# Kernel tuning notes

Measured on AMD Instinct MI355X. Metric: run time of the kernel, lower is better.

Reference implementation:

```python
import jax, jax.numpy as jnp
import numpy as np

N = 50000
E = 800000
IN_DIM = 128
HID = 32
HEADS = 8
OUT_DIM = 64
BN_EPS = 1e-5
NEG_SLOPE = 0.2


def batch_norm(x, gamma, beta, mean, var):
    # eval-mode BatchNorm1d using running statistics
    return (x - mean) * jax.lax.rsqrt(var + BN_EPS) * gamma + beta


def gat_conv(x, src, dst, W, att_src, att_dst, heads, out_ch, n):
    """PyG GATConv (shared src/dst lin), self-loops already included in src/dst.
    x: [n, in]; W: [in, heads*out_ch]; att_*: [heads, out_ch].
    Returns [n, heads, out_ch]."""
    h = (x @ W).reshape(n, heads, out_ch)                       # node features per head
    a_s = jnp.einsum('nho,ho->nh', h, att_src)                  # [n, heads]
    a_d = jnp.einsum('nho,ho->nh', h, att_dst)
    e = jax.nn.leaky_relu(a_s[src] + a_d[dst], NEG_SLOPE)       # [e, heads]
    # segment softmax over incoming edges of each dst node
    mx = jax.ops.segment_max(e, dst, num_segments=n)
    ex = jnp.exp(e - mx[dst])
    denom = jax.ops.segment_sum(ex, dst, num_segments=n)
    alpha = ex / (denom[dst] + 1e-16)                           # [e, heads]
    out = jax.ops.segment_sum(alpha[:, :, None] * h[src], dst, num_segments=n)
    return out                                                  # [n, heads, out_ch]


def setup_inputs() -> dict:
    key = jax.random.key(0)
    ks = jax.random.split(key, 24)
    inp = {}
    inp['x'] = jax.random.normal(ks[0], (N, IN_DIM), dtype=jnp.float32)
    inp['edge_index'] = jax.random.randint(ks[1], (2, E), 0, N, dtype=jnp.int64)
    s = 0.05
    inp['W1'] = jax.random.normal(ks[2], (IN_DIM, HEADS * HID), dtype=jnp.float32) * s
    inp['a_src1'] = jax.random.normal(ks[3], (HEADS, HID), dtype=jnp.float32) * s
    inp['a_dst1'] = jax.random.normal(ks[4], (HEADS, HID), dtype=jnp.float32) * s
    inp['b1'] = jnp.zeros((HEADS * HID,), dtype=jnp.float32)
    inp['W2'] = jax.random.normal(ks[5], (HEADS * HID, OUT_DIM), dtype=jnp.float32) * s
    inp['a_src2'] = jax.random.normal(ks[6], (1, OUT_DIM), dtype=jnp.float32) * s
    inp['a_dst2'] = jax.random.normal(ks[7], (1, OUT_DIM), dtype=jnp.float32) * s
    inp['b2'] = jnp.zeros((OUT_DIM,), dtype=jnp.float32)
    # projection Linear(out_dim -> in_dim)
    inp['Wp'] = jax.random.normal(ks[8], (OUT_DIM, IN_DIM), dtype=jnp.float32) * s
    inp['bp'] = jnp.zeros((IN_DIM,), dtype=jnp.float32)
    # BatchNorm params (eval mode running stats)
    for i, d in [(1, HEADS * HID), (2, OUT_DIM), (3, IN_DIM)]:
        k0, k1, k2, k3 = jax.random.split(ks[8 + i], 4)
        inp[f'g{i}'] = 1.0 + 0.1 * jax.random.normal(k0, (d,), dtype=jnp.float32)
        inp[f'be{i}'] = 0.1 * jax.random.normal(k1, (d,), dtype=jnp.float32)
        inp[f'm{i}'] = 0.1 * jax.random.normal(k2, (d,), dtype=jnp.float32)
        inp[f'v{i}'] = jax.random.uniform(k3, (d,), dtype=jnp.float32, minval=0.5, maxval=1.5)
    return inp


def reference(x, edge_index, W1, a_src1, a_dst1, b1, W2, a_src2, a_dst2, b2,
              Wp, bp, g1, be1, m1, v1, g2, be2, m2, v2, g3, be3, m3, v3):
    n = x.shape[0]
    loops = jnp.arange(n, dtype=edge_index.dtype)
    src = jnp.concatenate([edge_index[0], loops])   # add_self_loops=True (PyG default)
    dst = jnp.concatenate([edge_index[1], loops])

    h = gat_conv(x, src, dst, W1, a_src1, a_dst1, HEADS, HID, n)
    h = h.reshape(n, HEADS * HID) + b1              # concat=True
    h = jax.nn.elu(batch_norm(h, g1, be1, m1, v1))  # dropout is no-op in eval

    h = gat_conv(h, src, dst, W2, a_src2, a_dst2, 1, OUT_DIM, n)
    h = h.reshape(n, OUT_DIM) + b2                  # concat=False, heads=1 -> mean == identity
    h = jax.nn.elu(batch_norm(h, g2, be2, m2, v2))

    h = h @ Wp + bp
    return batch_norm(h, g3, be3, m3, v3)
```

## Files before the change

kernel.cpp:

```cpp
#include <hip/hip_runtime.h>
#include <math.h>

#define NEG_SLOPE 0.2f
#define BN_EPS 1e-5f

typedef __bf16 bf16x8 __attribute__((ext_vector_type(8)));
typedef float  f32x4  __attribute__((ext_vector_type(4)));

__device__ __forceinline__ float elu_f(float x){ return x > 0.f ? x : expm1f(x); }
__device__ __forceinline__ float lrelu_f(float x){ return x > 0.f ? x : NEG_SLOPE * x; }

__device__ __forceinline__ float b2f(ushort u){
    union { uint i; float f; } v; v.i = (uint)u << 16; return v.f;
}
__device__ __forceinline__ ushort f2b(float f){
    union { float f; uint i; } v; v.f = f;
    uint r = v.i + 0x7FFFu + ((v.i >> 16) & 1u);
    return (ushort)(r >> 16);
}

__device__ __forceinline__ bool detect_f64(const void* ei, int E, long long N)
{
    const long long* p = (const long long*)ei;
    int lane = threadIdx.x & 63;
    long long v = p[lane % max(1, min(2 * E, 64))];
    bool bad = (v < 0 || v >= N);
    return __ballot(bad) == 0ull;
}

__device__ __forceinline__ void get_edge(const void* ei, int e, int E, bool f64, int& s, int& d)
{
    if (e < E) {
        if (f64) { const long long* p = (const long long*)ei; s = (int)p[e]; d = (int)p[E + e]; }
        else     { const int*       p = (const int*)ei;       s = p[e];      d = p[E + e]; }
    } else {
        s = d = e - E;
    }
}

__global__ void setup_kernel(const void* ei, int E, int N, int* deg,
    const float* __restrict__ W1, const float* __restrict__ W2, const float* __restrict__ Wp,
    ushort* __restrict__ wt1, ushort* __restrict__ wt2, ushort* __restrict__ wtp,
    const float* b1, const float* b2, const float* bp,
    const float* g1, const float* be1, const float* m1, const float* v1,
    const float* g2, const float* be2, const float* m2, const float* v2,
    const float* g3, const float* be3, const float* m3, const float* v3,
    float* par)
{
    int b = blockIdx.x, t = threadIdx.x;
    if (b == 0) {
        { float s = g1[t] * rsqrtf(v1[t] + BN_EPS); par[t] = s;        par[256 + t] = b1[t] * s + be1[t] - m1[t] * s; }
        if (t < 64)  { float s = g2[t] * rsqrtf(v2[t] + BN_EPS); par[512 + t] = s;  par[576 + t] = b2[t] * s + be2[t] - m2[t] * s; }
        if (t < 128) { float s = g3[t] * rsqrtf(v3[t] + BN_EPS); par[640 + t] = s;  par[768 + t] = bp[t] * s + be3[t] - m3[t] * s; }
    } else if (b <= 224) {
        int idx = (b - 1) * 256 + t;
        if (idx < 32768) {
            int n = idx >> 7, k = idx & 127;
            wt1[idx] = f2b(W1[k * 256 + n]);
        } else if (idx < 49152) {
            int j = idx - 32768;
            int n = j >> 8, k = j & 255;
            wt2[j] = f2b(W2[k * 64 + n]);
        } else if (idx < 57344) {
            int j = idx - 49152;
            int n = j >> 6, k = j & 63;
            wtp[j] = f2b(Wp[k * 128 + n]);
        }
    } else {
        bool f64 = detect_f64(ei, E, (long long)N);
        int i = (b - 225) * 256 + t;
        int ET = E + N;
        if (i < ET) {
            int s, d;
            get_edge(ei, i, E, f64, s, d);
            atomicAdd(&deg[d], 1);
        }
    }
}

__global__ void scan1_kernel(const int* __restrict__ deg, int N, int* __restrict__ bsum)
{
    int b = blockIdx.x, t = threadIdx.x;
    int base = b * 4096 + t * 16;
    int s = 0;
    #pragma unroll
    for (int k = 0; k < 16; k += 4) {
        int idx = base + k;
        if (idx + 3 < N) {
            int4 v = *reinterpret_cast<const int4*>(&deg[idx]);
            s += v.x + v.y + v.z + v.w;
        } else {
            for (int q = 0; q < 4; ++q) if (idx + q < N) s += deg[idx + q];
        }
    }
    #pragma unroll
    for (int off = 1; off < 64; off <<= 1) s += __shfl_xor(s, off);
    __shared__ int wsum[4];
    if ((t & 63) == 0) wsum[t >> 6] = s;
    __syncthreads();
    if (t == 0) bsum[b] = wsum[0] + wsum[1] + wsum[2] + wsum[3];
}

__global__ void scan2_kernel(const int* __restrict__ bsum, int nb, int* __restrict__ bpre)
{
    if (threadIdx.x == 0) {
        int r = 0;
        for (int i = 0; i < nb; ++i) { bpre[i] = r; r += bsum[i]; }
        bpre[nb] = r;
    }
}

__global__ void scan3_kernel(const int* __restrict__ deg, int N,
                             const int* __restrict__ bpre, int nb,
                             int* __restrict__ rowptr, int* __restrict__ fillptr)
{
    int b = blockIdx.x, t = threadIdx.x;
    int base = b * 4096 + t * 16;
    int loc[16];
    int s = 0;
    #pragma unroll
    for (int k = 0; k < 16; ++k) {
        int idx = base + k;
        int d = (idx < N) ? deg[idx] : 0;
        loc[k] = s; s += d;
    }
    int lane = t & 63;
    int incl = s;
    #pragma unroll
    for (int off = 1; off < 64; off <<= 1) {
        int v = __shfl_up(incl, off);
        if (lane >= off) incl += v;
    }
    __shared__ int wsum[4];
    if (lane == 63) wsum[t >> 6] = incl;
    __syncthreads();
    int woff = 0;
    int w = t >> 6;
    for (int i = 0; i < w; ++i) woff += wsum[i];
    int off0 = bpre[b] + woff + incl - s;
    #pragma unroll
    for (int k = 0; k < 16; ++k) {
        int idx = base + k;
        if (idx < N) { rowptr[idx] = off0 + loc[k]; fillptr[idx] = off0 + loc[k]; }
    }
    if (b == 0 && t == 0) rowptr[N] = bpre[nb];
}

__global__ void fill_kernel(const void* ei, int E, int N, int* fillptr, int* esrc)
{
    bool f64 = detect_f64(ei, E, (long long)N);
    int i = blockIdx.x * blockDim.x + threadIdx.x;
    int ET = E + N;
    if (i >= ET) return;
    int s, d;
    get_edge(ei, i, E, f64, s, d);
    int pos = atomicAdd(&fillptr[d], 1);
    esrc[pos] = s;
}

template<int ATYPE, int OMODE, int ATT>
__global__ __launch_bounds__(256) void mgemm_kernel(const void* __restrict__ Ap,
    const ushort* __restrict__ Bt, void* __restrict__ Cp, int M, int K, int NC,
    const float* __restrict__ S, const float* __restrict__ Cc,
    const float* __restrict__ att_s, const float* __restrict__ att_d,
    float* __restrict__ as_out, float* __restrict__ ad_out)
{
    const int BM = 128, LDA = 72;
    __shared__ __align__(16) ushort As[BM][LDA];
    __shared__ __align__(16) ushort Bs[64][LDA];
    __shared__ float red[128][2];
    int t = threadIdx.x;
    int m0 = blockIdx.x * BM, n0 = blockIdx.y * 64;
    int w = t >> 6, l = t & 63;
    int wm = w >> 1, wn = w & 1;
    int r16 = l & 15, kg = l >> 4;

    f32x4 acc[4][2];
    #pragma unroll
    for (int mi = 0; mi < 4; ++mi)
        #pragma unroll
        for (int ni = 0; ni < 2; ++ni)
            acc[mi][ni] = (f32x4){0.f, 0.f, 0.f, 0.f};

    for (int kb = 0; kb < K; kb += 64) {
        if (ATYPE == 0) {
            const float* A = (const float*)Ap;
            #pragma unroll
            for (int p = 0; p < 8; ++p) {
                int r = (t >> 4) + p * 16, c4 = (t & 15) * 4;
                int gm = m0 + r;
                float4 v = (gm < M) ? *reinterpret_cast<const float4*>(&A[(size_t)gm * K + kb + c4])
                                    : make_float4(0.f, 0.f, 0.f, 0.f);
                ushort4 u; u.x = f2b(v.x); u.y = f2b(v.y); u.z = f2b(v.z); u.w = f2b(v.w);
                *reinterpret_cast<ushort4*>(&As[r][c4]) = u;
            }
        } else {
            const ushort* A = (const ushort*)Ap;
            #pragma unroll
            for (int p = 0; p < 4; ++p) {
                int r = (t >> 3) + p * 32, c8 = (t & 7) * 8;
                int gm = m0 + r;
                uint4 v = (gm < M) ? *reinterpret_cast<const uint4*>(&A[(size_t)gm * K + kb + c8])
                                   : make_uint4(0u, 0u, 0u, 0u);
                *reinterpret_cast<uint4*>(&As[r][c8]) = v;
            }
        }
        #pragma unroll
        for (int p = 0; p < 2; ++p) {
            int r = (t >> 3) + p * 32, c8 = (t & 7) * 8;
            uint4 v = *reinterpret_cast<const uint4*>(&Bt[(size_t)(n0 + r) * K + kb + c8]);
            *reinterpret_cast<uint4*>(&Bs[r][c8]) = v;
        }
        __syncthreads();
        #pragma unroll
        for (int kk = 0; kk < 2; ++kk) {
            bf16x8 bB[2], bA[4];
            #pragma unroll
            for (int ni = 0; ni < 2; ++ni)
                bB[ni] = *reinterpret_cast<const bf16x8*>(&Bs[wn * 32 + ni * 16 + r16][kk * 32 + kg * 8]);
            #pragma unroll
            for (int mi = 0; mi < 4; ++mi)
                bA[mi] = *reinterpret_cast<const bf16x8*>(&As[wm * 64 + mi * 16 + r16][kk * 32 + kg * 8]);
            #pragma unroll
            for (int mi = 0; mi < 4; ++mi)
                #pragma unroll
                for (int ni = 0; ni < 2; ++ni)
                    acc[mi][ni] = __builtin_amdgcn_mfma_f32_16x16x32_bf16(bA[mi], bB[ni], acc[mi][ni], 0, 0, 0);
        }
        __syncthreads();
    }
    #pragma unroll
    for (int mi = 0; mi < 4; ++mi) {
        #pragma unroll
        for (int ni = 0; ni < 2; ++ni) {
            #pragma unroll
            for (int rg = 0; rg < 4; ++rg) {
                int gm = m0 + wm * 64 + mi * 16 + kg * 4 + rg;
                int gc = n0 + wn * 32 + ni * 16 + r16;
                if (gm < M) {
                    float v = acc[mi][ni][rg];
                    if (OMODE == 0) ((ushort*)Cp)[(size_t)gm * NC + gc] = f2b(v);
                    else            ((float*)Cp)[(size_t)gm * NC + gc] = v * S[gc] + Cc[gc];
                }
            }
        }
    }
    if (ATT) {
        float cs0 = att_s[n0 + wn * 32 + r16], cs1 = att_s[n0 + wn * 32 + 16 + r16];
        float cd0 = att_d[n0 + wn * 32 + r16], cd1 = att_d[n0 + wn * 32 + 16 + r16];
        float sp[4][4], dp[4][4];
        #pragma unroll
        for (int mi = 0; mi < 4; ++mi)
            #pragma unroll
            for (int rg = 0; rg < 4; ++rg) {
                sp[mi][rg] = acc[mi][0][rg] * cs0 + acc[mi][1][rg] * cs1;
                dp[mi][rg] = acc[mi][0][rg] * cd0 + acc[mi][1][rg] * cd1;
            }
        #pragma unroll
        for (int off = 1; off < 16; off <<= 1)
            #pragma unroll
            for (int mi = 0; mi < 4; ++mi)
                #pragma unroll
                for (int rg = 0; rg < 4; ++rg) {
                    sp[mi][rg] += __shfl_xor(sp[mi][rg], off);
                    dp[mi][rg] += __shfl_xor(dp[mi][rg], off);
                }
        if (ATT == 1) {
            int head = (n0 >> 5) + wn;
            if (r16 == 0) {
                #pragma unroll
                for (int mi = 0; mi < 4; ++mi)
                    #pragma unroll
                    for (int rg = 0; rg < 4; ++rg) {
                        int gm = m0 + wm * 64 + mi * 16 + kg * 4 + rg;
                        if (gm < M) {
                            as_out[gm * 8 + head] = sp[mi][rg];
                            ad_out[gm * 8 + head] = dp[mi][rg];
                        }
                    }
            }
        } else {
            if (wn == 1 && r16 == 0) {
                #pragma unroll
                for (int mi = 0; mi < 4; ++mi)
                    #pragma unroll
                    for (int rg = 0; rg < 4; ++rg) {
                        int r = wm * 64 + mi * 16 + kg * 4 + rg;
                        red[r][0] = sp[mi][rg];
                        red[r][1] = dp[mi][rg];
                    }
            }
            __syncthreads();
            if (wn == 0 && r16 == 0) {
                #pragma unroll
                for (int mi = 0; mi < 4; ++mi)
                    #pragma unroll
                    for (int rg = 0; rg < 4; ++rg) {
                        int r = wm * 64 + mi * 16 + kg * 4 + rg;
                        int gm = m0 + r;
                        if (gm < M) {
                            as_out[gm] = sp[mi][rg] + red[r][0];
                            ad_out[gm] = dp[mi][rg] + red[r][1];
                        }
                    }
            }
        }
    }
}

__global__ void agg1_kernel(const ushort* __restrict__ h1,
                            const float* __restrict__ as1, const float* __restrict__ ad1,
                            const int* __restrict__ rowptr, const int* __restrict__ esrc,
                            const float* __restrict__ par,
                            ushort* __restrict__ outb, int N)
{
    __shared__ float wlds_all[4][64 * 8];
    float* wlds = wlds_all[threadIdx.x >> 6];
    int wid = (blockIdx.x * blockDim.x + threadIdx.x) >> 6;
    int lane = threadIdx.x & 63;
    if (wid >= N) return;
    int beg = rowptr[wid], end = rowptr[wid + 1];
    int h = lane & 7, j = lane >> 3;
    int li = lane & 31, half = lane >> 5, hh = li >> 2;
    float ad_h = ad1[wid * 8 + h];
    float den = 0.f;
    float acc[8] = {0.f, 0.f, 0.f, 0.f, 0.f, 0.f, 0.f, 0.f};

    for (int cb = beg; cb < end; cb += 64) {
        int ce = min(cb + 64, end);
        for (int i = cb + j; i < ce; i += 8) {
            float wv = __expf(lrelu_f(as1[esrc[i] * 8 + h] + ad_h));
            wlds[(i - cb) * 8 + h] = wv;
            den += wv;
        }
        __builtin_amdgcn_wave_barrier();
        auto edge1 = [&](int ii) {
            int src = esrc[ii];
            float al = wlds[(ii - cb) * 8 + hh];
            uint4 r = *reinterpret_cast<const uint4*>(&h1[(size_t)src * 256 + li * 8]);
            union { uint u; float f; } c0, c1;
            c0.u = r.x << 16; c1.u = r.x & 0xffff0000u; acc[0] += al * c0.f; acc[1] += al * c1.f;
            c0.u = r.y << 16; c1.u = r.y & 0xffff0000u; acc[2] += al * c0.f; acc[3] += al * c1.f;
            c0.u = r.z << 16; c1.u = r.z & 0xffff0000u; acc[4] += al * c0.f; acc[5] += al * c1.f;
            c0.u = r.w << 16; c1.u = r.w & 0xffff0000u; acc[6] += al * c0.f; acc[7] += al * c1.f;
        };
        int i = cb + half;
        for (; i + 6 < ce; i += 8) { edge1(i); edge1(i + 2); edge1(i + 4); edge1(i + 6); }
        for (; i < ce; i += 2) edge1(i);
        __builtin_amdgcn_wave_barrier();
    }

    den += __shfl_xor(den, 8, 64);
    den += __shfl_xor(den, 16, 64);
    den += __shfl_xor(den, 32, 64);
    float inv = 1.f / (den + 1e-16f);
    float inv_h = __shfl(inv, hh, 64);

    #pragma unroll
    for (int f = 0; f < 8; ++f) acc[f] += __shfl_xor(acc[f], 32, 64);
    if (half == 0) {
        int f0 = li * 8;
        const float* S1 = par;
        const float* C1 = par + 256;
        ushort o[8];
        #pragma unroll
        for (int f = 0; f < 8; ++f) o[f] = f2b(elu_f(acc[f] * inv_h * S1[f0 + f] + C1[f0 + f]));
        uint4 pk;
        pk.x = (uint)o[0] | ((uint)o[1] << 16);
        pk.y = (uint)o[2] | ((uint)o[3] << 16);
        pk.z = (uint)o[4] | ((uint)o[5] << 16);
        pk.w = (uint)o[6] | ((uint)o[7] << 16);
        *reinterpret_cast<uint4*>(&outb[(size_t)wid * 256 + f0]) = pk;
    }
}

__global__ void agg2_kernel(const ushort* __restrict__ h2,
                            const float* __restrict__ as2, const float* __restrict__ ad2,
                            const int* __restrict__ rowptr, const int* __restrict__ esrc,
                            const float* __restrict__ par,
                            ushort* __restrict__ outb, int N)
{
    __shared__ float wlds_all[4][64];
    float* wlds = wlds_all[threadIdx.x >> 6];
    int wid = (blockIdx.x * blockDim.x + threadIdx.x) >> 6;
    int lane = threadIdx.x & 63;
    if (wid >= N) return;
    int beg = rowptr[wid], end = rowptr[wid + 1];
    int li = lane & 31, half = lane >> 5;
    float ad = ad2[wid];
    float den = 0.f;
    float a0 = 0.f, a1 = 0.f;

    for (int cb = beg; cb < end; cb += 64) {
        int ce = min(cb + 64, end);
        {
            int i = cb + lane;
            if (i < ce) {
                float wv = __expf(lrelu_f(as2[esrc[i]] + ad));
                wlds[i - cb] = wv;
                den += wv;
            }
        }
        __builtin_amdgcn_wave_barrier();
        auto edge1 = [&](int ii) {
            int src = esrc[ii];
            float al = wlds[ii - cb];
            uint hv = *reinterpret_cast<const uint*>(&h2[(size_t)src * 64 + li * 2]);
            union { uint u; float f; } c0, c1;
            c0.u = hv << 16; c1.u = hv & 0xffff0000u;
            a0 += al * c0.f; a1 += al * c1.f;
        };
        int i = cb + half;
        for (; i + 6 < ce; i += 8) { edge1(i); edge1(i + 2); edge1(i + 4); edge1(i + 6); }
        for (; i < ce; i += 2) edge1(i);
        __builtin_amdgcn_wave_barrier();
    }

    #pragma unroll
    for (int off = 1; off < 64; off <<= 1) den += __shfl_xor(den, off, 64);
    float inv = 1.f / (den + 1e-16f);
    a0 += __shfl_xor(a0, 32, 64);
    a1 += __shfl_xor(a1, 32, 64);
    if (half == 0) {
        int f = li * 2;
        const float* S2 = par + 512;
        const float* C2 = par + 576;
        ushort2 o;
        o.x = f2b(elu_f(a0 * inv * S2[f] + C2[f]));
        o.y = f2b(elu_f(a1 * inv * S2[f + 1] + C2[f + 1]));
        *reinterpret_cast<ushort2*>(&outb[(size_t)wid * 64 + f]) = o;
    }
}

extern "C" void kernel_launch(void* const* d_in, const int* in_sizes, int n_in,
                              void* d_out, int out_size, void* d_ws, size_t ws_size,
                              hipStream_t stream)
{
    const float* x      = (const float*)d_in[0];
    const void*  ei     = d_in[1];
    const float* W1     = (const float*)d_in[2];
    const float* a_src1 = (const float*)d_in[3];
    const float* a_dst1 = (const float*)d_in[4];
    const float* b1     = (const float*)d_in[5];
    const float* W2     = (const float*)d_in[6];
    const float* a_src2 = (const float*)d_in[7];
    const float* a_dst2 = (const float*)d_in[8];
    const float* b2     = (const float*)d_in[9];
    const float* Wp     = (const float*)d_in[10];
    const float* bp     = (const float*)d_in[11];
    const float* g1 = (const float*)d_in[12], *be1 = (const float*)d_in[13];
    const float* m1 = (const float*)d_in[14], *v1  = (const float*)d_in[15];
    const float* g2 = (const float*)d_in[16], *be2 = (const float*)d_in[17];
    const float* m2 = (const float*)d_in[18], *v2  = (const float*)d_in[19];
    const float* g3 = (const float*)d_in[20], *be3 = (const float*)d_in[21];
    const float* m3 = (const float*)d_in[22], *v3  = (const float*)d_in[23];
    float* out = (float*)d_out;

    const int N  = in_sizes[0] / 128;
    const int E  = in_sizes[1] / 2;
    const int ET = E + N;

    char* base = (char*)d_ws;
    size_t off = 0;
    auto alloc = [&](size_t bytes) -> char* {
        char* p = base + off;
        off += (bytes + 255) & ~(size_t)255;
        return p;
    };
    float*  par     = (float*)alloc(1024 * 4);
    int*    bsum    = (int*)alloc(256);
    int*    bpre    = (int*)alloc(256);
    int*    rowptr  = (int*)alloc((size_t)(N + 1) * 4);
    int*    fillptr = (int*)alloc((size_t)(N + 1) * 4);
    int*    esrc    = (int*)alloc((size_t)ET * 4);
    float*  as1     = (float*)alloc((size_t)N * 8 * 4);
    float*  ad1     = (float*)alloc((size_t)N * 8 * 4);
    float*  as2     = (float*)alloc((size_t)N * 4);
    float*  ad2     = (float*)alloc((size_t)N * 4);
    ushort* wt1     = (ushort*)alloc(256 * 128 * 2);
    ushort* wt2     = (ushort*)alloc(64 * 256 * 2);
    ushort* wtp     = (ushort*)alloc(128 * 64 * 2);
    ushort* h1      = (ushort*)alloc((size_t)N * 256 * 2);
    ushort* h1b     = (ushort*)alloc((size_t)N * 256 * 2);
    ushort* h2      = (ushort*)alloc((size_t)N * 64 * 2);
    ushort* g2buf   = (ushort*)alloc((size_t)N * 64 * 2);

    hipMemsetAsync(fillptr, 0, (N + 1) * sizeof(int), stream);
    int cblocks = (ET + 255) / 256;
    setup_kernel<<<225 + cblocks, 256, 0, stream>>>(ei, E, N, fillptr,
        W1, W2, Wp, wt1, wt2, wtp,
        b1, b2, bp, g1, be1, m1, v1, g2, be2, m2, v2, g3, be3, m3, v3, par);

    int nb = (N + 4095) / 4096;
    scan1_kernel<<<nb, 256, 0, stream>>>(fillptr, N, bsum);
    scan2_kernel<<<1, 64, 0, stream>>>(bsum, nb, bpre);
    scan3_kernel<<<nb, 256, 0, stream>>>(fillptr, N, bpre, nb, rowptr, fillptr);
    fill_kernel<<<cblocks, 256, 0, stream>>>(ei, E, N, fillptr, esrc);

    int mb128 = (N + 127) / 128;
    int wbl   = (N + 3) / 4;
    mgemm_kernel<0, 0, 1><<<dim3(mb128, 4), 256, 0, stream>>>(x, wt1, h1, N, 128, 256,
        nullptr, nullptr, a_src1, a_dst1, as1, ad1);
    agg1_kernel<<<wbl, 256, 0, stream>>>(h1, as1, ad1, rowptr, esrc, par, h1b, N);

    mgemm_kernel<1, 0, 2><<<dim3(mb128, 1), 256, 0, stream>>>(h1b, wt2, h2, N, 256, 64,
        nullptr, nullptr, a_src2, a_dst2, as2, ad2);
    agg2_kernel<<<wbl, 256, 0, stream>>>(h2, as2, ad2, rowptr, esrc, par, g2buf, N);

    mgemm_kernel<1, 1, 0><<<dim3(mb128, 2), 256, 0, stream>>>(g2buf, wtp, out, N, 64, 128,
        par + 640, par + 768, nullptr, nullptr, nullptr, nullptr);
}
```

Measured before the change: 292.1 us.

## Pre-convert x to bf16 and batch gathers via LDS-staged source indices

Adds a bf16 conversion of x inside the setup kernel, so the first GEMM reads bf16 input instead of fp32, which is re-read across four column blocks. In both aggregation kernels, source indices are cached in LDS during the weight pass, and the feature gather loop issues eight independent loads before consuming them to raise memory-level parallelism. The cost is an extra pass over x (fp32 read plus bf16 write) and higher register pressure from the unrolled load buffers.

```diff
diff --git a/kernel.cpp b/kernel.cpp
--- a/kernel.cpp
+++ b/kernel.cpp
@@ -38,7 +38,8 @@
     }
 }
 
-__global__ void setup_kernel(const void* ei, int E, int N, int* deg,
+__global__ void setup_kernel(const void* ei, int E, int N, int* deg, int cx,
+    const float* __restrict__ x, ushort* __restrict__ xb,
     const float* __restrict__ W1, const float* __restrict__ W2, const float* __restrict__ Wp,
     ushort* __restrict__ wt1, ushort* __restrict__ wt2, ushort* __restrict__ wtp,
     const float* b1, const float* b2, const float* bp,
@@ -66,9 +67,26 @@
             int n = j >> 6, k = j & 63;
             wtp[j] = f2b(Wp[k * 128 + n]);
         }
+    } else if (b < 225 + cx) {
+        long long n128 = (long long)N * 128;
+        long long idx = ((long long)(b - 225) * 256 + t) * 8;
+        if (idx + 7 < n128) {
+            float4 v0 = *reinterpret_cast<const float4*>(&x[idx]);
+            float4 v1 = *reinterpret_cast<const float4*>(&x[idx + 4]);
+            ushort o[8] = { f2b(v0.x), f2b(v0.y), f2b(v0.z), f2b(v0.w),
+                            f2b(v1.x), f2b(v1.y), f2b(v1.z), f2b(v1.w) };
+            uint4 pk;
+            pk.x = (uint)o[0] | ((uint)o[1] << 16);
+            pk.y = (uint)o[2] | ((uint)o[3] << 16);
+            pk.z = (uint)o[4] | ((uint)o[5] << 16);
+            pk.w = (uint)o[6] | ((uint)o[7] << 16);
+            *reinterpret_cast<uint4*>(&xb[idx]) = pk;
+        } else {
+            for (long long q = idx; q < n128; ++q) xb[q] = f2b(x[q]);
+        }
     } else {
         bool f64 = detect_f64(ei, E, (long long)N);
-        int i = (b - 225) * 256 + t;
+        int i = (b - 225 - cx) * 256 + t;
         int ET = E + N;
         if (i < ET) {
             int s, d;
@@ -315,7 +333,9 @@
                             ushort* __restrict__ outb, int N)
 {
     __shared__ float wlds_all[4][64 * 8];
+    __shared__ int   slds_all[4][64];
     float* wlds = wlds_all[threadIdx.x >> 6];
+    int*   slds = slds_all[threadIdx.x >> 6];
     int wid = (blockIdx.x * blockDim.x + threadIdx.x) >> 6;
     int lane = threadIdx.x & 63;
     if (wid >= N) return;
@@ -329,15 +349,14 @@
     for (int cb = beg; cb < end; cb += 64) {
         int ce = min(cb + 64, end);
         for (int i = cb + j; i < ce; i += 8) {
-            float wv = __expf(lrelu_f(as1[esrc[i] * 8 + h] + ad_h));
+            int src = esrc[i];
+            float wv = __expf(lrelu_f(as1[src * 8 + h] + ad_h));
             wlds[(i - cb) * 8 + h] = wv;
+            if (h == 0) slds[i - cb] = src;
             den += wv;
         }
         __builtin_amdgcn_wave_barrier();
-        auto edge1 = [&](int ii) {
-            int src = esrc[ii];
-            float al = wlds[(ii - cb) * 8 + hh];
-            uint4 r = *reinterpret_cast<const uint4*>(&h1[(size_t)src * 256 + li * 8]);
+        auto fma1 = [&](uint4 r, float al) {
             union { uint u; float f; } c0, c1;
             c0.u = r.x << 16; c1.u = r.x & 0xffff0000u; acc[0] += al * c0.f; acc[1] += al * c1.f;
             c0.u = r.y << 16; c1.u = r.y & 0xffff0000u; acc[2] += al * c0.f; acc[3] += al * c1.f;
@@ -345,8 +364,22 @@
             c0.u = r.w << 16; c1.u = r.w & 0xffff0000u; acc[6] += al * c0.f; acc[7] += al * c1.f;
         };
         int i = cb + half;
-        for (; i + 6 < ce; i += 8) { edge1(i); edge1(i + 2); edge1(i + 4); edge1(i + 6); }
-        for (; i < ce; i += 2) edge1(i);
+        for (; i + 14 < ce; i += 16) {
+            uint4 r[8];
+            #pragma unroll
+            for (int q = 0; q < 8; ++q) {
+                int src = slds[i + q * 2 - cb];
+                r[q] = *reinterpret_cast<const uint4*>(&h1[(size_t)src * 256 + li * 8]);
+            }
+            #pragma unroll
+            for (int q = 0; q < 8; ++q)
+                fma1(r[q], wlds[(i + q * 2 - cb) * 8 + hh]);
+        }
+        for (; i < ce; i += 2) {
+            int src = slds[i - cb];
+            uint4 r = *reinterpret_cast<const uint4*>(&h1[(size_t)src * 256 + li * 8]);
+            fma1(r, wlds[(i - cb) * 8 + hh]);
+        }
         __builtin_amdgcn_wave_barrier();
     }
 
@@ -381,7 +414,9 @@
                             ushort* __restrict__ outb, int N)
 {
     __shared__ float wlds_all[4][64];
+    __shared__ int   slds_all[4][64];
     float* wlds = wlds_all[threadIdx.x >> 6];
+    int*   slds = slds_all[threadIdx.x >> 6];
     int wid = (blockIdx.x * blockDim.x + threadIdx.x) >> 6;
     int lane = threadIdx.x & 63;
     if (wid >= N) return;
@@ -396,23 +431,36 @@
         {
             int i = cb + lane;
             if (i < ce) {
-                float wv = __expf(lrelu_f(as2[esrc[i]] + ad));
+                int src = esrc[i];
+                float wv = __expf(lrelu_f(as2[src] + ad));
                 wlds[i - cb] = wv;
+                slds[i - cb] = src;
                 den += wv;
             }
         }
         __builtin_amdgcn_wave_barrier();
-        auto edge1 = [&](int ii) {
-            int src = esrc[ii];
-            float al = wlds[ii - cb];
-            uint hv = *reinterpret_cast<const uint*>(&h2[(size_t)src * 64 + li * 2]);
+        auto fma1 = [&](uint hv, float al) {
             union { uint u; float f; } c0, c1;
             c0.u = hv << 16; c1.u = hv & 0xffff0000u;
             a0 += al * c0.f; a1 += al * c1.f;
         };
         int i = cb + half;
-        for (; i + 6 < ce; i += 8) { edge1(i); edge1(i + 2); edge1(i + 4); edge1(i + 6); }
-        for (; i < ce; i += 2) edge1(i);
+        for (; i + 14 < ce; i += 16) {
+            uint r[8];
+            #pragma unroll
+            for (int q = 0; q < 8; ++q) {
+                int src = slds[i + q * 2 - cb];
+                r[q] = *reinterpret_cast<const uint*>(&h2[(size_t)src * 64 + li * 2]);
+            }
+            #pragma unroll
+            for (int q = 0; q < 8; ++q)
+                fma1(r[q], wlds[i + q * 2 - cb]);
+        }
+        for (; i < ce; i += 2) {
+            int src = slds[i - cb];
+            uint r = *reinterpret_cast<const uint*>(&h2[(size_t)src * 64 + li * 2]);
+            fma1(r, wlds[i - cb]);
+        }
         __builtin_amdgcn_wave_barrier();
     }
 
@@ -480,15 +528,17 @@
     ushort* wt1     = (ushort*)alloc(256 * 128 * 2);
     ushort* wt2     = (ushort*)alloc(64 * 256 * 2);
     ushort* wtp     = (ushort*)alloc(128 * 64 * 2);
+    ushort* xb      = (ushort*)alloc((size_t)N * 128 * 2);
     ushort* h1      = (ushort*)alloc((size_t)N * 256 * 2);
     ushort* h1b     = (ushort*)alloc((size_t)N * 256 * 2);
     ushort* h2      = (ushort*)alloc((size_t)N * 64 * 2);
     ushort* g2buf   = (ushort*)alloc((size_t)N * 64 * 2);
 
     hipMemsetAsync(fillptr, 0, (N + 1) * sizeof(int), stream);
+    int cx = (int)(((size_t)N * 128 + 2047) / 2048);
     int cblocks = (ET + 255) / 256;
-    setup_kernel<<<225 + cblocks, 256, 0, stream>>>(ei, E, N, fillptr,
-        W1, W2, Wp, wt1, wt2, wtp,
+    setup_kernel<<<225 + cx + cblocks, 256, 0, stream>>>(ei, E, N, fillptr, cx,
+        x, xb, W1, W2, Wp, wt1, wt2, wtp,
         b1, b2, bp, g1, be1, m1, v1, g2, be2, m2, v2, g3, be3, m3, v3, par);
 
     int nb = (N + 4095) / 4096;
@@ -499,7 +549,7 @@
 
     int mb128 = (N + 127) / 128;
     int wbl   = (N + 3) / 4;
-    mgemm_kernel<0, 0, 1><<<dim3(mb128, 4), 256, 0, stream>>>(x, wt1, h1, N, 128, 256,
+    mgemm_kernel<1, 0, 1><<<dim3(mb128, 4), 256, 0, stream>>>(xb, wt1, h1, N, 128, 256,
         nullptr, nullptr, a_src1, a_dst1, as1, ad1);
     agg1_kernel<<<wbl, 256, 0, stream>>>(h1, as1, ad1, rowptr, esrc, par, h1b, N);
 
```

Result: slower. 307.5 us (+5.3%).
